# Optimization experiments

Measured on AMD Instinct MI355X. Metric: run time of the kernel, lower is better.

The kernel has to match this reference:

```python
import jax, jax.numpy as jnp
import numpy as np

B, L, NSTATE = 8192, 256, 9


def setup_inputs() -> dict:
    key = jax.random.key(0)
    k1, k2, k3, k4 = jax.random.split(key, 4)
    inputs = jax.random.normal(k1, (B, L, NSTATE), dtype=jnp.float32)
    path = jax.random.randint(k2, (B, L), 0, NSTATE, dtype=jnp.int32)
    # learned CRF params (init'd to zeros in the module; use small random for a
    # non-degenerate reference)
    tran = jax.random.normal(k3, (NSTATE, NSTATE), dtype=jnp.float32) * 0.1
    init = jax.random.normal(k4, (NSTATE,), dtype=jnp.float32) * 0.1
    return {"inputs": inputs, "path": path, "tran": tran, "init": init}


def reference(inputs, path, tran, init):
    # inputs: [B, L, S], path: [B, L], tran: [S, S], init: [S]
    # bio=False -> mask and imask are all zeros (no-op additions).
    # --- gold path score ---
    emit = jnp.take_along_axis(inputs, path[..., None], axis=-1)[..., 0]  # [B, L]
    tran_sc = tran[path[..., :-1], path[..., 1:]]                         # [B, L-1]
    path_scores = emit.sum(-1) + init[path[..., 0]] + tran_sc.sum(-1)     # [B]

    # --- partition function via log-semiring forward recurrence ---
    alpha0 = init + inputs[..., 0, :]                                     # [B, S]

    def step(alpha, x_t):
        # alpha: [B, S] (prev state), x_t: [B, S] (emission at t)
        nxt = alpha[..., :, None] + tran + x_t[..., None, :]              # [B, S, S]
        return jax.nn.logsumexp(nxt, axis=-2), None

    xs = jnp.moveaxis(inputs[..., 1:, :], -2, 0)                          # [L-1, B, S]
    alpha, _ = jax.lax.scan(step, alpha0, xs)
    scores = jax.nn.logsumexp(alpha, axis=-1)                             # [B]
    return scores - path_scores
```

## Files before the change

### kernel.cpp

```cpp
#include <hip/hip_runtime.h>


#define B_N 8192
#define L_N 256
#define SEQ_STRIDE 2304
#define HALF 128
#define SPB 6
#define XW 54
#define XSTRIDE 55
#define PLS 129
#define SPW 16
#define NDIR_BLOCKS (B_N / SPW)

#define LOG2E 1.44269504088896340736f
#define LN2f  0.69314718055994530942f

#define QP1 57
#define QP2 78
#define QP3 147
#define QROT(src, CTRL) \
  __int_as_float(__builtin_amdgcn_mov_dpp(__float_as_int(src), CTRL, 0xf, 0xf, 0))

#define WAITV0  asm volatile("s_waitcnt vmcnt(0)" ::: "memory")
#define WAITV16 asm volatile("s_waitcnt vmcnt(16)" ::: "memory")

__device__ __forceinline__ void gl_lds4(const void* g, void* l) {
  __builtin_amdgcn_global_load_lds(
      (const __attribute__((address_space(1))) void*)g,
      (__attribute__((address_space(3))) void*)l, 4, 0, 0);
}

__device__ __forceinline__ float fexp(float x) {
  return __builtin_amdgcn_exp2f(x * LOG2E);
}

#define FWD_STEP_BODY(KK, EA, DO_RESC)                                      \
  do {                                                                      \
    float g[4][3];                                                          \
    _Pragma("unroll") for (int k = 0; k < 3; ++k) {                         \
      g[0][k] = o[k];                                                       \
      g[1][k] = QROT(o[k], QP1);                                            \
      g[2][k] = QROT(o[k], QP2);                                            \
      g[3][k] = QROT(o[k], QP3);                                            \
    }                                                                       \
    if (DO_RESC) {                                                          \
      float m = g[0][0];                                                    \
      _Pragma("unroll") for (int r = 0; r < 4; ++r)                         \
        _Pragma("unroll") for (int k = 0; k < 3; ++k)                       \
          m = fmaxf(m, g[r][k]);                                            \
      const int ex = (int)((__float_as_uint(m) >> 23) & 0xffu) - 126;       \
      ce += ex;                                                             \
      const float sc = __uint_as_float((unsigned)(127 - ex) << 23);         \
      _Pragma("unroll") for (int r = 0; r < 4; ++r)                         \
        _Pragma("unroll") for (int k = 0; k < 3; ++k)                       \
          g[r][k] *= sc;                                                    \
    }                                                                       \
    float out3[3];                                                          \
    _Pragma("unroll") for (int i = 0; i < 3; ++i) {                         \
      float a = Erot[0][0][i] * g[0][0];                                    \
      _Pragma("unroll") for (int r = 0; r < 4; ++r)                         \
        _Pragma("unroll") for (int k = 0; k < 3; ++k)                       \
          if (r + k > 0) a = fmaf(Erot[r][k][i], g[r][k], a);               \
      out3[i] = a;                                                          \
    }                                                                       \
    _Pragma("unroll") for (int i = 0; i < 3; ++i)                           \
      o[i] = out3[i] * EA[(KK) * 3 + i];                                    \
  } while (0)

#define BWD_STEP_BODY(KK, EA, DO_RESC)                                      \
  do {                                                                      \
    const int tt_ = 5 - (KK);                                               \
    float wv[3];                                                            \
    _Pragma("unroll") for (int k = 0; k < 3; ++k)                           \
      wv[k] = EA[tt_ * 3 + k] * o[k];                                       \
    float g[4][3];                                                          \
    _Pragma("unroll") for (int k = 0; k < 3; ++k) {                         \
      g[0][k] = wv[k];                                                      \
      g[1][k] = QROT(wv[k], QP1);                                           \
      g[2][k] = QROT(wv[k], QP2);                                           \
      g[3][k] = QROT(wv[k], QP3);                                           \
    }                                                                       \
    if (DO_RESC) {                                                          \
      float m = g[0][0];                                                    \
      _Pragma("unroll") for (int r = 0; r < 4; ++r)                         \
        _Pragma("unroll") for (int k = 0; k < 3; ++k)                       \
          m = fmaxf(m, g[r][k]);                                            \
      const int ex = (int)((__float_as_uint(m) >> 23) & 0xffu) - 126;       \
      ce += ex;                                                             \
      const float sc = __uint_as_float((unsigned)(127 - ex) << 23);         \
      _Pragma("unroll") for (int r = 0; r < 4; ++r)                         \
        _Pragma("unroll") for (int k = 0; k < 3; ++k)                       \
          g[r][k] *= sc;                                                    \
    }                                                                       \
    float out3[3];                                                          \
    _Pragma("unroll") for (int i = 0; i < 3; ++i) {                         \
      float a = Erot[0][0][i] * g[0][0];                                    \
      _Pragma("unroll") for (int r = 0; r < 4; ++r)                         \
        _Pragma("unroll") for (int k = 0; k < 3; ++k)                       \
          if (r + k > 0) a = fmaf(Erot[r][k][i], g[r][k], a);               \
      out3[i] = a;                                                          \
    }                                                                       \
    _Pragma("unroll") for (int i = 0; i < 3; ++i) o[i] = out3[i];           \
  } while (0)

#define PREFETCH_WIN(NB)                                                    \
  if (lane < XW) {                                                          \
    const int fb = fwd ? (NB) * XW : (SEQ_STRIDE - XW * ((NB) + 1));        \
    float* dst = &lx[(NB) % 3][0];                                          \
    _Pragma("unroll") for (int r = 0; r < SPW; ++r)                         \
      gl_lds4(xg + (size_t)(seq0 + r) * SEQ_STRIDE + fb + lane,             \
              dst + r * XSTRIDE);                                           \
  }

#define EBATCH_TO(EA, LXQ)                                                  \
  _Pragma("unroll") for (int tt = 0; tt < 6; ++tt)                          \
    _Pragma("unroll") for (int k = 0; k < 3; ++k)                           \
      EA[tt * 3 + k] = fexp((LXQ)[tt * 9 + myoff + k]);

#define EMTR_FWD_TO(EMA, TRA, LXQ, PCA, PPREV)                              \
  _Pragma("unroll") for (int kk = 0; kk < 6; ++kk) {                        \
    EMA[kk] = (LXQ)[kk * 9 + PCA[kk]];                                      \
    const int pp_ = kk ? PCA[kk - 1] : (PPREV);                             \
    TRA[kk] = ltran[pp_ * 9 + PCA[kk]];                                     \
  }

#define EMTR_BWD_TO(EMA, TRA, LXQ, PCA, PPREV)                              \
  _Pragma("unroll") for (int kk = 0; kk < 6; ++kk) {                        \
    const int pc_ = kk ? PCA[kk - 1] : (PPREV);                             \
    EMA[kk] = (LXQ)[(5 - kk) * 9 + pc_];                                    \
    TRA[kk] = ltran[PCA[kk] * 9 + pc_];                                     \
  }

#define PREREAD_TO(PNA, TBN)                                                \
  if (fwd) {                                                                \
    _Pragma("unroll") for (int kk = 0; kk < 6; ++kk) {                      \
      int t_ = (TBN) + kk; if (t_ > HALF - 1) t_ = HALF - 1;                \
      PNA[kk] = plr[t_];                                                    \
    }                                                                       \
  } else {                                                                  \
    _Pragma("unroll") for (int kk = 0; kk < 6; ++kk) {                      \
      int idx_ = 127 - (TBN) - kk; if (idx_ < 0) idx_ = 0;                  \
      PNA[kk] = plr[idx_];                                                  \
    }                                                                       \
  }

#define ROTATE_NEXT                                                         \
  _Pragma("unroll") for (int j = 0; j < 18; ++j) eC[j] = eN[j];             \
  _Pragma("unroll") for (int j = 0; j < 6; ++j) {                           \
    emC[j] = emN[j]; trC[j] = trN[j]; pcC[j] = pcN[j]; pcN[j] = pnN[j];     \
  }

__global__ __launch_bounds__(64, 1) void crf_half(
    const float* __restrict__ xg, const int* __restrict__ path,
    const float* __restrict__ tran, const float* __restrict__ initv,
    float* __restrict__ ws)
{
  __shared__ float lx[3][SPW * XSTRIDE];
  __shared__ int   pl[SPW * PLS];
  __shared__ int   pl255[SPW];
  __shared__ float ltran[81];

  const int lane = threadIdx.x;
  const int c = lane & 3;
  const int q = lane >> 2;
  const bool fwd = (int)blockIdx.x < NDIR_BLOCKS;
  const int seq0 = (fwd ? blockIdx.x : blockIdx.x - NDIR_BLOCKS) * SPW;

  for (int i = lane; i < 81; i += 64) ltran[i] = tran[i];
  if (!fwd && lane < SPW)
    pl255[lane] = path[(size_t)(seq0 + lane) * L_N + 255];

  {
    const int t0 = fwd ? 0 : 127;
#pragma unroll
    for (int r = 0; r < SPW; ++r) {
      const int* g = path + (size_t)(seq0 + r) * L_N + t0 + lane;
      gl_lds4(g,      &pl[r * PLS]);
      gl_lds4(g + 64, &pl[r * PLS + 64]);
    }
  }
  if (lane < XW) {
#pragma unroll
    for (int wi = 0; wi < 2; ++wi) {
      const int fb = fwd ? wi * XW : (SEQ_STRIDE - XW * (wi + 1));
#pragma unroll
      for (int r = 0; r < SPW; ++r)
        gl_lds4(xg + (size_t)(seq0 + r) * SEQ_STRIDE + fb + lane,
                &lx[wi][r * XSTRIDE]);
    }
  }

  float Erot[4][3][3];
#pragma unroll
  for (int r = 0; r < 4; ++r)
#pragma unroll
    for (int k = 0; k < 3; ++k)
#pragma unroll
      for (int i = 0; i < 3; ++i) {
        const int ig = 3 * c + i;
        const int jg = 3 * ((c + r) & 3) + k;
        float v = 0.f;
        if (ig < 9 && jg < 9)
          v = fexp(fwd ? tran[jg * 9 + ig] : tran[ig * 9 + jg]);
        Erot[r][k][i] = v;
      }

  float iv[3];
#pragma unroll
  for (int k = 0; k < 3; ++k) {
    iv[k] = (fwd && c < 3) ? initv[3 * c + k] : 0.f;
    asm volatile("" :: "v"(iv[k]));
  }

  float o[3];
  float emit = 0.f, trn = 0.f;
  int ce = 0, pcur = 0;
  if (!fwd) {
#pragma unroll
    for (int k = 0; k < 3; ++k) o[k] = (c < 3) ? 1.f : 0.f;
  }

  const int myoff = (c == 3) ? 0 : 3 * c;
  const int* plr = &pl[q * PLS];

  WAITV0;
  if (!fwd) pcur = pl255[q];

  int pcC[6], pcN[6];
  if (fwd) {
#pragma unroll
    for (int kk = 0; kk < 6; ++kk) pcC[kk] = plr[kk];
  } else {
#pragma unroll
    for (int kk = 0; kk < 6; ++kk) pcC[kk] = plr[127 - kk];
  }
  float eC[18], emC[6], trC[6];
  {
    const float* lxq0 = &lx[0][q * XSTRIDE];
    EBATCH_TO(eC, lxq0)
    if (fwd) { EMTR_FWD_TO(emC, trC, lxq0, pcC, pcur) }
    else     { EMTR_BWD_TO(emC, trC, lxq0, pcC, pcur) }
  }
  float xv0[3];
#pragma unroll
  for (int k = 0; k < 3; ++k) xv0[k] = lx[0][q * XSTRIDE + myoff + k];
  PREREAD_TO(pcN, SPB)

  {
    PREFETCH_WIN(2)
    WAITV16;
    const float* lxqN = &lx[1][q * XSTRIDE];
    float eN[18], emN[6], trN[6]; int pnN[6];
    EBATCH_TO(eN, lxqN)
    if (fwd) { EMTR_FWD_TO(emN, trN, lxqN, pcN, pcC[5]) }
    else     { EMTR_BWD_TO(emN, trN, lxqN, pcN, pcC[5]) }
    PREREAD_TO(pnN, 2 * SPB)
    if (fwd) {
#pragma unroll
      for (int k = 0; k < 3; ++k)
        o[k] = (c < 3) ? fexp(iv[k] + xv0[k]) : 0.f;
      FWD_STEP_BODY(1, eC, false);
      FWD_STEP_BODY(2, eC, false);
      FWD_STEP_BODY(3, eC, false);
      FWD_STEP_BODY(4, eC, false);
      FWD_STEP_BODY(5, eC, false);
#pragma unroll
      for (int kk = 0; kk < 6; ++kk) emit += emC[kk];
#pragma unroll
      for (int kk = 1; kk < 6; ++kk) trn += trC[kk];
    } else {
      BWD_STEP_BODY(0, eC, false);
      BWD_STEP_BODY(1, eC, false);
      BWD_STEP_BODY(2, eC, false);
      BWD_STEP_BODY(3, eC, false);
      BWD_STEP_BODY(4, eC, false);
      BWD_STEP_BODY(5, eC, false);
#pragma unroll
      for (int kk = 0; kk < 6; ++kk) { emit += emC[kk]; trn += trC[kk]; }
    }
    ROTATE_NEXT
  }

#pragma unroll 1
  for (int b = 1; b <= 20; ++b) {
    if (b + 2 <= 21) {
      PREFETCH_WIN(b + 2)
      WAITV16;
    } else {
      WAITV0;
    }
    const float* lxqN = &lx[(b + 1) % 3][q * XSTRIDE];
    float eN[18], emN[6], trN[6]; int pnN[6];
    EBATCH_TO(eN, lxqN)
    if (fwd) { EMTR_FWD_TO(emN, trN, lxqN, pcN, pcC[5]) }
    else     { EMTR_BWD_TO(emN, trN, lxqN, pcN, pcC[5]) }
    PREREAD_TO(pnN, (b + 2) * SPB)
    if (fwd) {
      FWD_STEP_BODY(0, eC, true);
      FWD_STEP_BODY(1, eC, false);
      FWD_STEP_BODY(2, eC, false);
      FWD_STEP_BODY(3, eC, false);
      FWD_STEP_BODY(4, eC, false);
      FWD_STEP_BODY(5, eC, false);
    } else {
      BWD_STEP_BODY(0, eC, true);
      BWD_STEP_BODY(1, eC, false);
      BWD_STEP_BODY(2, eC, false);
      BWD_STEP_BODY(3, eC, false);
      BWD_STEP_BODY(4, eC, false);
      BWD_STEP_BODY(5, eC, false);
    }
#pragma unroll
    for (int kk = 0; kk < 6; ++kk) { emit += emC[kk]; trn += trC[kk]; }
    ROTATE_NEXT
  }

  {
    if (fwd) {
      FWD_STEP_BODY(0, eC, true);
      FWD_STEP_BODY(1, eC, false);
    } else {
      BWD_STEP_BODY(0, eC, true);
      BWD_STEP_BODY(1, eC, false);
    }
#pragma unroll
    for (int kk = 0; kk < 2; ++kk) { emit += emC[kk]; trn += trC[kk]; }
  }

  const int sq = seq0 + q;
  float* wp = ws + sq;
  if (fwd) {
    if (c < 3) {
#pragma unroll
      for (int k = 0; k < 3; ++k) wp[(3 * c + k) * B_N] = o[k];
    } else {
      wp[9 * B_N] = (float)ce;
      wp[10 * B_N] = emit + trn + initv[plr[0]];
    }
  } else {
    if (c < 3) {
#pragma unroll
      for (int k = 0; k < 3; ++k) wp[(11 + 3 * c + k) * B_N] = o[k];
    } else {
      wp[20 * B_N] = (float)ce;
      wp[21 * B_N] = emit + trn;
    }
  }
}

__global__ __launch_bounds__(256) void crf_combine(
    const float* __restrict__ ws, float* __restrict__ out)
{
  const int s = blockIdx.x * 256 + threadIdx.x;
  float dot = 0.f;
#pragma unroll
  for (int i = 0; i < 9; ++i)
    dot = fmaf(ws[i * B_N + s], ws[(11 + i) * B_N + s], dot);
  const float score =
      (__builtin_amdgcn_logf(dot) + ws[9 * B_N + s] + ws[20 * B_N + s]) * LN2f;
  out[s] = score - (ws[10 * B_N + s] + ws[21 * B_N + s]);
}

extern "C" void kernel_launch(void* const* d_in, const int* in_sizes, int n_in,
                              void* d_out, int out_size, void* d_ws, size_t ws_size,
                              hipStream_t stream) {
  (void)in_sizes; (void)n_in; (void)out_size; (void)ws_size;
  const float* xg    = (const float*)d_in[0];
  const int*   path  = (const int*)d_in[1];
  const float* tran  = (const float*)d_in[2];
  const float* initv = (const float*)d_in[3];
  float* ws  = (float*)d_ws;
  float* out = (float*)d_out;

  crf_half<<<2 * NDIR_BLOCKS, 64, 0, stream>>>(xg, path, tran, initv, ws);
  crf_combine<<<B_N / 256, 256, 0, stream>>>(ws, out);
}
```

Measured before the change: 126.9 us.

## Fuse forward and backward halves into one wave and drop combine kernel

Each wave now runs both the forward and the backward half-recurrence for its 16 sequences, interleaving the two independent dependency chains step by step, and combines the results in registers with a DPP reduction. This removes the workspace round-trip and the second combine launch. The x windows move from triple to double buffering with a full vmcnt(0) wait per block. The change halves the grid to 512 single-wave blocks and roughly doubles register pressure per thread, trading TLP for ILP.

```diff
diff --git a/kernel.cpp b/kernel.cpp
--- a/kernel.cpp
+++ b/kernel.cpp
@@ -8,9 +8,9 @@
 #define SPB 6
 #define XW 54
 #define XSTRIDE 55
-#define PLS 129
+#define PLS 257
 #define SPW 16
-#define NDIR_BLOCKS (B_N / SPW)
+#define NBLOCKS (B_N / SPW)
 
 #define LOG2E 1.44269504088896340736f
 #define LN2f  0.69314718055994530942f
@@ -18,11 +18,11 @@
 #define QP1 57
 #define QP2 78
 #define QP3 147
+#define QPX1 177
 #define QROT(src, CTRL) \
   __int_as_float(__builtin_amdgcn_mov_dpp(__float_as_int(src), CTRL, 0xf, 0xf, 0))
 
-#define WAITV0  asm volatile("s_waitcnt vmcnt(0)" ::: "memory")
-#define WAITV16 asm volatile("s_waitcnt vmcnt(16)" ::: "memory")
+#define WAITV0 asm volatile("s_waitcnt vmcnt(0)" ::: "memory")
 
 __device__ __forceinline__ void gl_lds4(const void* g, void* l) {
   __builtin_amdgcn_global_load_lds(
@@ -34,14 +34,14 @@
   return __builtin_amdgcn_exp2f(x * LOG2E);
 }
 
-#define FWD_STEP_BODY(KK, EA, DO_RESC)                                      \
+#define FSTEP(KK, DO_RESC)                                                  \
   do {                                                                      \
     float g[4][3];                                                          \
     _Pragma("unroll") for (int k = 0; k < 3; ++k) {                         \
-      g[0][k] = o[k];                                                       \
-      g[1][k] = QROT(o[k], QP1);                                            \
-      g[2][k] = QROT(o[k], QP2);                                            \
-      g[3][k] = QROT(o[k], QP3);                                            \
+      g[0][k] = of[k];                                                      \
+      g[1][k] = QROT(of[k], QP1);                                           \
+      g[2][k] = QROT(of[k], QP2);                                           \
+      g[3][k] = QROT(of[k], QP3);                                           \
     }                                                                       \
     if (DO_RESC) {                                                          \
       float m = g[0][0];                                                    \
@@ -49,7 +49,7 @@
         _Pragma("unroll") for (int k = 0; k < 3; ++k)                       \
           m = fmaxf(m, g[r][k]);                                            \
       const int ex = (int)((__float_as_uint(m) >> 23) & 0xffu) - 126;       \
-      ce += ex;                                                             \
+      ce_f += ex;                                                           \
       const float sc = __uint_as_float((unsigned)(127 - ex) << 23);         \
       _Pragma("unroll") for (int r = 0; r < 4; ++r)                         \
         _Pragma("unroll") for (int k = 0; k < 3; ++k)                       \
@@ -57,22 +57,22 @@
     }                                                                       \
     float out3[3];                                                          \
     _Pragma("unroll") for (int i = 0; i < 3; ++i) {                         \
-      float a = Erot[0][0][i] * g[0][0];                                    \
-      _Pragma("unroll") for (int r = 0; r < 4; ++r)                         \
-        _Pragma("unroll") for (int k = 0; k < 3; ++k)                       \
-          if (r + k > 0) a = fmaf(Erot[r][k][i], g[r][k], a);               \
+      float a = Erf[0][0][i] * g[0][0];                                     \
+      _Pragma("unroll") for (int r = 0; r < 4; ++r)                         \
+        _Pragma("unroll") for (int k = 0; k < 3; ++k)                       \
+          if (r + k > 0) a = fmaf(Erf[r][k][i], g[r][k], a);                \
       out3[i] = a;                                                          \
     }                                                                       \
     _Pragma("unroll") for (int i = 0; i < 3; ++i)                           \
-      o[i] = out3[i] * EA[(KK) * 3 + i];                                    \
+      of[i] = out3[i] * eCf[(KK) * 3 + i];                                  \
   } while (0)
 
-#define BWD_STEP_BODY(KK, EA, DO_RESC)                                      \
+#define BSTEP(KK, DO_RESC)                                                  \
   do {                                                                      \
     const int tt_ = 5 - (KK);                                               \
     float wv[3];                                                            \
     _Pragma("unroll") for (int k = 0; k < 3; ++k)                           \
-      wv[k] = EA[tt_ * 3 + k] * o[k];                                       \
+      wv[k] = eCb[tt_ * 3 + k] * ob[k];                                     \
     float g[4][3];                                                          \
     _Pragma("unroll") for (int k = 0; k < 3; ++k) {                         \
       g[0][k] = wv[k];                                                      \
@@ -86,7 +86,7 @@
         _Pragma("unroll") for (int k = 0; k < 3; ++k)                       \
           m = fmaxf(m, g[r][k]);                                            \
       const int ex = (int)((__float_as_uint(m) >> 23) & 0xffu) - 126;       \
-      ce += ex;                                                             \
+      ce_b += ex;                                                           \
       const float sc = __uint_as_float((unsigned)(127 - ex) << 23);         \
       _Pragma("unroll") for (int r = 0; r < 4; ++r)                         \
         _Pragma("unroll") for (int k = 0; k < 3; ++k)                       \
@@ -94,19 +94,27 @@
     }                                                                       \
     float out3[3];                                                          \
     _Pragma("unroll") for (int i = 0; i < 3; ++i) {                         \
-      float a = Erot[0][0][i] * g[0][0];                                    \
-      _Pragma("unroll") for (int r = 0; r < 4; ++r)                         \
-        _Pragma("unroll") for (int k = 0; k < 3; ++k)                       \
-          if (r + k > 0) a = fmaf(Erot[r][k][i], g[r][k], a);               \
+      float a = Erb[0][0][i] * g[0][0];                                     \
+      _Pragma("unroll") for (int r = 0; r < 4; ++r)                         \
+        _Pragma("unroll") for (int k = 0; k < 3; ++k)                       \
+          if (r + k > 0) a = fmaf(Erb[r][k][i], g[r][k], a);                \
       out3[i] = a;                                                          \
     }                                                                       \
-    _Pragma("unroll") for (int i = 0; i < 3; ++i) o[i] = out3[i];           \
+    _Pragma("unroll") for (int i = 0; i < 3; ++i) ob[i] = out3[i];          \
   } while (0)
 
-#define PREFETCH_WIN(NB)                                                    \
+#define PREFETCH_F(NB)                                                      \
   if (lane < XW) {                                                          \
-    const int fb = fwd ? (NB) * XW : (SEQ_STRIDE - XW * ((NB) + 1));        \
-    float* dst = &lx[(NB) % 3][0];                                          \
+    const int fb = (NB) * XW;                                               \
+    float* dst = &lxf[(NB) & 1][0];                                         \
+    _Pragma("unroll") for (int r = 0; r < SPW; ++r)                         \
+      gl_lds4(xg + (size_t)(seq0 + r) * SEQ_STRIDE + fb + lane,             \
+              dst + r * XSTRIDE);                                           \
+  }
+#define PREFETCH_B(NB)                                                      \
+  if (lane < XW) {                                                          \
+    const int fb = SEQ_STRIDE - XW * ((NB) + 1);                            \
+    float* dst = &lxb[(NB) & 1][0];                                         \
     _Pragma("unroll") for (int r = 0; r < SPW; ++r)                         \
       gl_lds4(xg + (size_t)(seq0 + r) * SEQ_STRIDE + fb + lane,             \
               dst + r * XSTRIDE);                                           \
@@ -117,80 +125,66 @@
     _Pragma("unroll") for (int k = 0; k < 3; ++k)                           \
       EA[tt * 3 + k] = fexp((LXQ)[tt * 9 + myoff + k]);
 
-#define EMTR_FWD_TO(EMA, TRA, LXQ, PCA, PPREV)                              \
+#define EMTR_F(EMA, TRA, LXQ, PCA, PPREV)                                   \
   _Pragma("unroll") for (int kk = 0; kk < 6; ++kk) {                        \
     EMA[kk] = (LXQ)[kk * 9 + PCA[kk]];                                      \
     const int pp_ = kk ? PCA[kk - 1] : (PPREV);                             \
     TRA[kk] = ltran[pp_ * 9 + PCA[kk]];                                     \
   }
-
-#define EMTR_BWD_TO(EMA, TRA, LXQ, PCA, PPREV)                              \
+#define EMTR_B(EMA, TRA, LXQ, PCA, PPREV)                                   \
   _Pragma("unroll") for (int kk = 0; kk < 6; ++kk) {                        \
     const int pc_ = kk ? PCA[kk - 1] : (PPREV);                             \
     EMA[kk] = (LXQ)[(5 - kk) * 9 + pc_];                                    \
     TRA[kk] = ltran[PCA[kk] * 9 + pc_];                                     \
   }
 
-#define PREREAD_TO(PNA, TBN)                                                \
-  if (fwd) {                                                                \
-    _Pragma("unroll") for (int kk = 0; kk < 6; ++kk) {                      \
-      int t_ = (TBN) + kk; if (t_ > HALF - 1) t_ = HALF - 1;                \
-      PNA[kk] = plr[t_];                                                    \
-    }                                                                       \
-  } else {                                                                  \
-    _Pragma("unroll") for (int kk = 0; kk < 6; ++kk) {                      \
-      int idx_ = 127 - (TBN) - kk; if (idx_ < 0) idx_ = 0;                  \
-      PNA[kk] = plr[idx_];                                                  \
-    }                                                                       \
-  }
-
-#define ROTATE_NEXT                                                         \
-  _Pragma("unroll") for (int j = 0; j < 18; ++j) eC[j] = eN[j];             \
-  _Pragma("unroll") for (int j = 0; j < 6; ++j) {                           \
-    emC[j] = emN[j]; trC[j] = trN[j]; pcC[j] = pcN[j]; pcN[j] = pnN[j];     \
-  }
-
-__global__ __launch_bounds__(64, 1) void crf_half(
+#define PREREAD_F(PNA, TBN)                                                 \
+  _Pragma("unroll") for (int kk = 0; kk < 6; ++kk) {                        \
+    int t_ = (TBN) + kk; if (t_ > HALF - 1) t_ = HALF - 1;                  \
+    PNA[kk] = plr[t_];                                                      \
+  }
+#define PREREAD_B(PNA, TBN)                                                 \
+  _Pragma("unroll") for (int kk = 0; kk < 6; ++kk) {                        \
+    int idx_ = 254 - (TBN) - kk; if (idx_ < 127) idx_ = 127;                \
+    PNA[kk] = plr[idx_];                                                    \
+  }
+
+__global__ __launch_bounds__(64, 1) void crf_fused(
     const float* __restrict__ xg, const int* __restrict__ path,
     const float* __restrict__ tran, const float* __restrict__ initv,
-    float* __restrict__ ws)
+    float* __restrict__ out)
 {
-  __shared__ float lx[3][SPW * XSTRIDE];
+  __shared__ float lxf[2][SPW * XSTRIDE];
+  __shared__ float lxb[2][SPW * XSTRIDE];
   __shared__ int   pl[SPW * PLS];
-  __shared__ int   pl255[SPW];
   __shared__ float ltran[81];
 
   const int lane = threadIdx.x;
   const int c = lane & 3;
   const int q = lane >> 2;
-  const bool fwd = (int)blockIdx.x < NDIR_BLOCKS;
-  const int seq0 = (fwd ? blockIdx.x : blockIdx.x - NDIR_BLOCKS) * SPW;
+  const int seq0 = blockIdx.x * SPW;
 
   for (int i = lane; i < 81; i += 64) ltran[i] = tran[i];
-  if (!fwd && lane < SPW)
-    pl255[lane] = path[(size_t)(seq0 + lane) * L_N + 255];
-
-  {
-    const int t0 = fwd ? 0 : 127;
+
+#pragma unroll
+  for (int r = 0; r < SPW; ++r) {
+    const int* g = path + (size_t)(seq0 + r) * L_N + lane;
+    gl_lds4(g,       &pl[r * PLS]);
+    gl_lds4(g + 64,  &pl[r * PLS + 64]);
+    gl_lds4(g + 128, &pl[r * PLS + 128]);
+    gl_lds4(g + 192, &pl[r * PLS + 192]);
+  }
+  if (lane < XW) {
 #pragma unroll
     for (int r = 0; r < SPW; ++r) {
-      const int* g = path + (size_t)(seq0 + r) * L_N + t0 + lane;
-      gl_lds4(g,      &pl[r * PLS]);
-      gl_lds4(g + 64, &pl[r * PLS + 64]);
-    }
-  }
-  if (lane < XW) {
-#pragma unroll
-    for (int wi = 0; wi < 2; ++wi) {
-      const int fb = fwd ? wi * XW : (SEQ_STRIDE - XW * (wi + 1));
-#pragma unroll
-      for (int r = 0; r < SPW; ++r)
-        gl_lds4(xg + (size_t)(seq0 + r) * SEQ_STRIDE + fb + lane,
-                &lx[wi][r * XSTRIDE]);
-    }
-  }
-
-  float Erot[4][3][3];
+      gl_lds4(xg + (size_t)(seq0 + r) * SEQ_STRIDE + lane,
+              &lxf[0][r * XSTRIDE]);
+      gl_lds4(xg + (size_t)(seq0 + r) * SEQ_STRIDE + (SEQ_STRIDE - XW) + lane,
+              &lxb[0][r * XSTRIDE]);
+    }
+  }
+
+  float Erf[4][3][3], Erb[4][3][3];
 #pragma unroll
   for (int r = 0; r < 4; ++r)
 #pragma unroll
@@ -199,179 +193,160 @@
       for (int i = 0; i < 3; ++i) {
         const int ig = 3 * c + i;
         const int jg = 3 * ((c + r) & 3) + k;
-        float v = 0.f;
-        if (ig < 9 && jg < 9)
-          v = fexp(fwd ? tran[jg * 9 + ig] : tran[ig * 9 + jg]);
-        Erot[r][k][i] = v;
+        float vf = 0.f, vb = 0.f;
+        if (ig < 9 && jg < 9) {
+          vf = fexp(tran[jg * 9 + ig]);
+          vb = fexp(tran[ig * 9 + jg]);
+        }
+        Erf[r][k][i] = vf;
+        Erb[r][k][i] = vb;
       }
 
   float iv[3];
 #pragma unroll
   for (int k = 0; k < 3; ++k) {
-    iv[k] = (fwd && c < 3) ? initv[3 * c + k] : 0.f;
+    iv[k] = (c < 3) ? initv[3 * c + k] : 0.f;
     asm volatile("" :: "v"(iv[k]));
   }
 
-  float o[3];
-  float emit = 0.f, trn = 0.f;
-  int ce = 0, pcur = 0;
-  if (!fwd) {
-#pragma unroll
-    for (int k = 0; k < 3; ++k) o[k] = (c < 3) ? 1.f : 0.f;
-  }
+  float of[3], ob[3];
+#pragma unroll
+  for (int k = 0; k < 3; ++k) ob[k] = (c < 3) ? 1.f : 0.f;
+  float emit_f = 0.f, trn_f = 0.f, emit_b = 0.f, trn_b = 0.f;
+  int ce_f = 0, ce_b = 0;
 
   const int myoff = (c == 3) ? 0 : 3 * c;
   const int* plr = &pl[q * PLS];
 
   WAITV0;
-  if (!fwd) pcur = pl255[q];
-
-  int pcC[6], pcN[6];
-  if (fwd) {
-#pragma unroll
-    for (int kk = 0; kk < 6; ++kk) pcC[kk] = plr[kk];
-  } else {
-#pragma unroll
-    for (int kk = 0; kk < 6; ++kk) pcC[kk] = plr[127 - kk];
-  }
-  float eC[18], emC[6], trC[6];
+
+  int pcur_f = 0;
+  int pcur_b = plr[255];
+  int pcf[6], pcb[6];
+  PREREAD_F(pcf, 0)
+  PREREAD_B(pcb, 0)
+
   {
-    const float* lxq0 = &lx[0][q * XSTRIDE];
-    EBATCH_TO(eC, lxq0)
-    if (fwd) { EMTR_FWD_TO(emC, trC, lxq0, pcC, pcur) }
-    else     { EMTR_BWD_TO(emC, trC, lxq0, pcC, pcur) }
-  }
-  float xv0[3];
-#pragma unroll
-  for (int k = 0; k < 3; ++k) xv0[k] = lx[0][q * XSTRIDE + myoff + k];
-  PREREAD_TO(pcN, SPB)
-
-  {
-    PREFETCH_WIN(2)
-    WAITV16;
-    const float* lxqN = &lx[1][q * XSTRIDE];
-    float eN[18], emN[6], trN[6]; int pnN[6];
-    EBATCH_TO(eN, lxqN)
-    if (fwd) { EMTR_FWD_TO(emN, trN, lxqN, pcN, pcC[5]) }
-    else     { EMTR_BWD_TO(emN, trN, lxqN, pcN, pcC[5]) }
-    PREREAD_TO(pnN, 2 * SPB)
-    if (fwd) {
-#pragma unroll
-      for (int k = 0; k < 3; ++k)
-        o[k] = (c < 3) ? fexp(iv[k] + xv0[k]) : 0.f;
-      FWD_STEP_BODY(1, eC, false);
-      FWD_STEP_BODY(2, eC, false);
-      FWD_STEP_BODY(3, eC, false);
-      FWD_STEP_BODY(4, eC, false);
-      FWD_STEP_BODY(5, eC, false);
-#pragma unroll
-      for (int kk = 0; kk < 6; ++kk) emit += emC[kk];
-#pragma unroll
-      for (int kk = 1; kk < 6; ++kk) trn += trC[kk];
-    } else {
-      BWD_STEP_BODY(0, eC, false);
-      BWD_STEP_BODY(1, eC, false);
-      BWD_STEP_BODY(2, eC, false);
-      BWD_STEP_BODY(3, eC, false);
-      BWD_STEP_BODY(4, eC, false);
-      BWD_STEP_BODY(5, eC, false);
-#pragma unroll
-      for (int kk = 0; kk < 6; ++kk) { emit += emC[kk]; trn += trC[kk]; }
-    }
-    ROTATE_NEXT
+    PREFETCH_F(1)
+    PREFETCH_B(1)
+    const float* lxqf = &lxf[0][q * XSTRIDE];
+    const float* lxqb = &lxb[0][q * XSTRIDE];
+    float eCf[18], eCb[18];
+    EBATCH_TO(eCf, lxqf)
+    EBATCH_TO(eCb, lxqb)
+    float emf[6], trf[6], emb[6], trb[6];
+    EMTR_F(emf, trf, lxqf, pcf, 0)
+    EMTR_B(emb, trb, lxqb, pcb, pcur_b)
+    int pnf[6], pnb[6];
+    PREREAD_F(pnf, SPB)
+    PREREAD_B(pnb, SPB)
+#pragma unroll
+    for (int k = 0; k < 3; ++k)
+      of[k] = (c < 3) ? fexp(iv[k] + lxqf[myoff + k]) : 0.f;
+    BSTEP(0, false);
+    FSTEP(1, false);  BSTEP(1, false);
+    FSTEP(2, false);  BSTEP(2, false);
+    FSTEP(3, false);  BSTEP(3, false);
+    FSTEP(4, false);  BSTEP(4, false);
+    FSTEP(5, false);  BSTEP(5, false);
+#pragma unroll
+    for (int kk = 0; kk < 6; ++kk) {
+      emit_f += emf[kk]; emit_b += emb[kk]; trn_b += trb[kk];
+    }
+#pragma unroll
+    for (int kk = 1; kk < 6; ++kk) trn_f += trf[kk];
+    pcur_f = pcf[5]; pcur_b = pcb[5];
+#pragma unroll
+    for (int kk = 0; kk < 6; ++kk) { pcf[kk] = pnf[kk]; pcb[kk] = pnb[kk]; }
   }
 
 #pragma unroll 1
   for (int b = 1; b <= 20; ++b) {
-    if (b + 2 <= 21) {
-      PREFETCH_WIN(b + 2)
-      WAITV16;
-    } else {
-      WAITV0;
-    }
-    const float* lxqN = &lx[(b + 1) % 3][q * XSTRIDE];
-    float eN[18], emN[6], trN[6]; int pnN[6];
-    EBATCH_TO(eN, lxqN)
-    if (fwd) { EMTR_FWD_TO(emN, trN, lxqN, pcN, pcC[5]) }
-    else     { EMTR_BWD_TO(emN, trN, lxqN, pcN, pcC[5]) }
-    PREREAD_TO(pnN, (b + 2) * SPB)
-    if (fwd) {
-      FWD_STEP_BODY(0, eC, true);
-      FWD_STEP_BODY(1, eC, false);
-      FWD_STEP_BODY(2, eC, false);
-      FWD_STEP_BODY(3, eC, false);
-      FWD_STEP_BODY(4, eC, false);
-      FWD_STEP_BODY(5, eC, false);
-    } else {
-      BWD_STEP_BODY(0, eC, true);
-      BWD_STEP_BODY(1, eC, false);
-      BWD_STEP_BODY(2, eC, false);
-      BWD_STEP_BODY(3, eC, false);
-      BWD_STEP_BODY(4, eC, false);
-      BWD_STEP_BODY(5, eC, false);
-    }
-#pragma unroll
-    for (int kk = 0; kk < 6; ++kk) { emit += emC[kk]; trn += trC[kk]; }
-    ROTATE_NEXT
+    const int tb = b * SPB;
+    WAITV0;
+    PREFETCH_F(b + 1)
+    PREFETCH_B(b + 1)
+    const float* lxqf = &lxf[b & 1][q * XSTRIDE];
+    const float* lxqb = &lxb[b & 1][q * XSTRIDE];
+    float eCf[18], eCb[18];
+    EBATCH_TO(eCf, lxqf)
+    EBATCH_TO(eCb, lxqb)
+    float emf[6], trf[6], emb[6], trb[6];
+    EMTR_F(emf, trf, lxqf, pcf, pcur_f)
+    EMTR_B(emb, trb, lxqb, pcb, pcur_b)
+    int pnf[6], pnb[6];
+    PREREAD_F(pnf, tb + SPB)
+    PREREAD_B(pnb, tb + SPB)
+    FSTEP(0, true);   BSTEP(0, true);
+    FSTEP(1, false);  BSTEP(1, false);
+    FSTEP(2, false);  BSTEP(2, false);
+    FSTEP(3, false);  BSTEP(3, false);
+    FSTEP(4, false);  BSTEP(4, false);
+    FSTEP(5, false);  BSTEP(5, false);
+#pragma unroll
+    for (int kk = 0; kk < 6; ++kk) {
+      emit_f += emf[kk]; trn_f += trf[kk];
+      emit_b += emb[kk]; trn_b += trb[kk];
+    }
+    pcur_f = pcf[5]; pcur_b = pcb[5];
+#pragma unroll
+    for (int kk = 0; kk < 6; ++kk) { pcf[kk] = pnf[kk]; pcb[kk] = pnb[kk]; }
   }
 
   {
-    if (fwd) {
-      FWD_STEP_BODY(0, eC, true);
-      FWD_STEP_BODY(1, eC, false);
-    } else {
-      BWD_STEP_BODY(0, eC, true);
-      BWD_STEP_BODY(1, eC, false);
-    }
-#pragma unroll
-    for (int kk = 0; kk < 2; ++kk) { emit += emC[kk]; trn += trC[kk]; }
-  }
-
-  const int sq = seq0 + q;
-  float* wp = ws + sq;
-  if (fwd) {
-    if (c < 3) {
-#pragma unroll
-      for (int k = 0; k < 3; ++k) wp[(3 * c + k) * B_N] = o[k];
-    } else {
-      wp[9 * B_N] = (float)ce;
-      wp[10 * B_N] = emit + trn + initv[plr[0]];
-    }
-  } else {
-    if (c < 3) {
-#pragma unroll
-      for (int k = 0; k < 3; ++k) wp[(11 + 3 * c + k) * B_N] = o[k];
-    } else {
-      wp[20 * B_N] = (float)ce;
-      wp[21 * B_N] = emit + trn;
-    }
-  }
-}
-
-__global__ __launch_bounds__(256) void crf_combine(
-    const float* __restrict__ ws, float* __restrict__ out)
-{
-  const int s = blockIdx.x * 256 + threadIdx.x;
-  float dot = 0.f;
-#pragma unroll
-  for (int i = 0; i < 9; ++i)
-    dot = fmaf(ws[i * B_N + s], ws[(11 + i) * B_N + s], dot);
+    WAITV0;
+    const float* lxqf = &lxf[1][q * XSTRIDE];
+    const float* lxqb = &lxb[1][q * XSTRIDE];
+    float eCf[18], eCb[18];
+#pragma unroll
+    for (int tt = 0; tt < 2; ++tt)
+#pragma unroll
+      for (int k = 0; k < 3; ++k)
+        eCf[tt * 3 + k] = fexp(lxqf[tt * 9 + myoff + k]);
+#pragma unroll
+    for (int tt = 4; tt < 6; ++tt)
+#pragma unroll
+      for (int k = 0; k < 3; ++k)
+        eCb[tt * 3 + k] = fexp(lxqb[tt * 9 + myoff + k]);
+    float emf[2], trf[2], emb[2], trb[2];
+#pragma unroll
+    for (int kk = 0; kk < 2; ++kk) {
+      emf[kk] = lxqf[kk * 9 + pcf[kk]];
+      const int pp_ = kk ? pcf[kk - 1] : pcur_f;
+      trf[kk] = ltran[pp_ * 9 + pcf[kk]];
+      const int pc_ = kk ? pcb[kk - 1] : pcur_b;
+      emb[kk] = lxqb[(5 - kk) * 9 + pc_];
+      trb[kk] = ltran[pcb[kk] * 9 + pc_];
+    }
+    FSTEP(0, true);   BSTEP(0, true);
+    FSTEP(1, false);  BSTEP(1, false);
+#pragma unroll
+    for (int kk = 0; kk < 2; ++kk) {
+      emit_f += emf[kk]; trn_f += trf[kk];
+      emit_b += emb[kk]; trn_b += trb[kk];
+    }
+  }
+
+  float pd = of[0] * ob[0] + of[1] * ob[1] + of[2] * ob[2];
+  pd += QROT(pd, QPX1);
+  pd += QROT(pd, QP2);
+  const float w10 = emit_f + trn_f + initv[plr[0]];
+  const float w21 = emit_b + trn_b;
   const float score =
-      (__builtin_amdgcn_logf(dot) + ws[9 * B_N + s] + ws[20 * B_N + s]) * LN2f;
-  out[s] = score - (ws[10 * B_N + s] + ws[21 * B_N + s]);
+      (__builtin_amdgcn_logf(pd) + (float)ce_f + (float)ce_b) * LN2f
+      - (w10 + w21);
+  if (c == 0) out[seq0 + q] = score;
 }
 
 extern "C" void kernel_launch(void* const* d_in, const int* in_sizes, int n_in,
                               void* d_out, int out_size, void* d_ws, size_t ws_size,
                               hipStream_t stream) {
-  (void)in_sizes; (void)n_in; (void)out_size; (void)ws_size;
+  (void)in_sizes; (void)n_in; (void)out_size; (void)d_ws; (void)ws_size;
   const float* xg    = (const float*)d_in[0];
   const int*   path  = (const int*)d_in[1];
   const float* tran  = (const float*)d_in[2];
   const float* initv = (const float*)d_in[3];
-  float* ws  = (float*)d_ws;
   float* out = (float*)d_out;
 
-  crf_half<<<2 * NDIR_BLOCKS, 64, 0, stream>>>(xg, path, tran, initv, ws);
-  crf_combine<<<B_N / 256, 256, 0, stream>>>(ws, out);
+  crf_fused<<<NBLOCKS, 64, 0, stream>>>(xg, path, tran, initv, out);
 }
```

Result: slower. 141.7 us (+11.6%).
